# Performance work log

Hardware: AMD Instinct MI355X
Metric: run time of the kernel (lower is better)

The kernel has to match this reference:

```python
import jax, jax.numpy as jnp
import numpy as np
import math

EPS = 1e-6
ROPE_BASE = 10000.0

def _rmsnorm(x, w):
    # normalize over last dim (head_dim)
    rms = jax.lax.rsqrt(jnp.mean(x * x, axis=-1, keepdims=True) + EPS)
    return x * rms * w

def _rope_cos_sin(seq_len, head_dim, dtype):
    inv_freq = 1.0 / (ROPE_BASE ** (jnp.arange(0, head_dim, 2, dtype=jnp.float32) / head_dim))
    t = jnp.arange(seq_len, dtype=jnp.float32)
    freqs = jnp.outer(t, inv_freq)            # [S, Dh/2]
    emb = jnp.concatenate([freqs, freqs], -1)  # [S, Dh]
    return jnp.cos(emb).astype(dtype), jnp.sin(emb).astype(dtype)

def _rotate_half(x):
    half = x.shape[-1] // 2
    return jnp.concatenate([-x[..., half:], x[..., :half]], axis=-1)

def setup_inputs() -> dict:
    key = jax.random.key(0)
    ks = jax.random.split(key, 6)
    B, S, E = 1, 2048, 2048
    H, KVH, Dh = 16, 4, 128
    x = jax.random.normal(ks[0], (B, S, E), dtype=jnp.float32)
    mask = jnp.triu(jnp.ones((S, S), dtype=bool), k=1)  # True = masked (causal)
    scale = 0.02
    Wq = jax.random.normal(ks[1], (E, E), dtype=jnp.float32) * scale
    Wk = jax.random.normal(ks[2], (KVH * Dh, E), dtype=jnp.float32) * scale
    Wv = jax.random.normal(ks[3], (KVH * Dh, E), dtype=jnp.float32) * scale
    Wo = jax.random.normal(ks[4], (E, E), dtype=jnp.float32) * scale
    q_norm_w = jnp.ones((Dh,), dtype=jnp.float32)
    k_norm_w = jnp.ones((Dh,), dtype=jnp.float32)
    return {"x": x, "mask": mask, "Wq": Wq, "Wk": Wk, "Wv": Wv, "Wo": Wo,
            "q_norm_w": q_norm_w, "k_norm_w": k_norm_w}

def reference(x, mask, Wq, Wk, Wv, Wo, q_norm_w, k_norm_w):
    B, S, E = x.shape
    H, Dh = 16, E // 16
    KVH = Wk.shape[0] // Dh
    rep = H // KVH
    # QKV projections (torch Linear: x @ W.T)
    q = (x @ Wq.T).reshape(B, S, H, Dh).transpose(0, 2, 1, 3)    # [B,H,S,Dh]
    k = (x @ Wk.T).reshape(B, S, KVH, Dh).transpose(0, 2, 1, 3)  # [B,KVH,S,Dh]
    v = (x @ Wv.T).reshape(B, S, KVH, Dh).transpose(0, 2, 1, 3)
    # QK-RMSNorm
    q = _rmsnorm(q, q_norm_w)
    k = _rmsnorm(k, k_norm_w)
    # RoPE
    cos, sin = _rope_cos_sin(S, Dh, q.dtype)  # [S,Dh]
    q = q * cos + _rotate_half(q) * sin
    k = k * cos + _rotate_half(k) * sin
    # GQA expand kv heads (repeat_interleave on head dim)
    k = jnp.repeat(k, rep, axis=1)  # [B,H,S,Dh]
    v = jnp.repeat(v, rep, axis=1)
    # SDPA (no yarn => scale = 1/sqrt(head_dim))
    scale = 1.0 / math.sqrt(Dh)
    scores = jnp.einsum('bhqd,bhkd->bhqk', q, k) * scale
    scores = jnp.where(mask[None, None, :, :], -jnp.inf, scores)
    attn = jax.nn.softmax(scores, axis=-1)
    attn = jnp.nan_to_num(attn, nan=0.0)
    out = jnp.einsum('bhqk,bhkd->bhqd', attn, v)
    out = out.transpose(0, 2, 1, 3).reshape(B, S, E)
    return out @ Wo.T
```

## Files before the change

kernel.cpp:

```cpp
#include <hip/hip_runtime.h>
#include <hip/hip_bf16.h>
#include <cstdint>
#include <cstddef>

using bf16 = __hip_bfloat16;
typedef __attribute__((ext_vector_type(8))) short short8;
typedef __attribute__((ext_vector_type(4))) float f32x4;

#define MFMA16(a, b, c) __builtin_amdgcn_mfma_f32_16x16x32_bf16((a), (b), (c), 0, 0, 0)

static constexpr int S = 2048;
static constexpr int E = 2048;
static constexpr int H = 16;
static constexpr int KVH = 4;
static constexpr int Dh = 128;
static constexpr int NQKV = 3072;
static constexpr float ATTN_SCALE = 0.08838834764831845f;
static constexpr float NEG_BIG = -1e30f;

__device__ __forceinline__ short f2bs(float f) {
  __hip_bfloat16 h = __float2bfloat16(f);
  return *reinterpret_cast<short*>(&h);
}

__device__ __forceinline__ unsigned int pack_bf16(float lo, float hi) {
  return ((unsigned int)(unsigned short)f2bs(hi) << 16) |
         (unsigned int)(unsigned short)f2bs(lo);
}

__device__ __forceinline__ void gload_lds16(const void* g, void* l) {
  __builtin_amdgcn_global_load_lds(
      (const __attribute__((address_space(1))) unsigned int*)g,
      (__attribute__((address_space(3))) unsigned int*)l,
      16, 0, 0);
}

__global__ void cvt_all(const float* __restrict__ x,  const float* __restrict__ wq,
                        const float* __restrict__ wk, const float* __restrict__ wv,
                        const float* __restrict__ wo,
                        bf16* __restrict__ xb, bf16* __restrict__ wcat,
                        bf16* __restrict__ wob) {
  const long M1 = 4l << 20, M2 = 8l << 20, M3 = 9l << 20, M4 = 10l << 20, M5 = 14l << 20;
  long i = ((long)blockIdx.x * 256 + threadIdx.x) * 8;
  if (i >= M5) return;
  const float* src;
  bf16* dst;
  if (i < M1)      { src = x  + i;        dst = xb + i; }
  else if (i < M2) { src = wq + (i - M1); dst = wcat + (i - M1); }
  else if (i < M3) { src = wk + (i - M2); dst = wcat + 2048l * 2048 + (i - M2); }
  else if (i < M4) { src = wv + (i - M3); dst = wcat + 2560l * 2048 + (i - M3); }
  else             { src = wo + (i - M4); dst = wob + (i - M4); }
  const float4* s4 = reinterpret_cast<const float4*>(src);
  float4 a = s4[0];
  float4 b = s4[1];
  short8 o;
  o[0] = f2bs(a.x); o[1] = f2bs(a.y); o[2] = f2bs(a.z); o[3] = f2bs(a.w);
  o[4] = f2bs(b.x); o[5] = f2bs(b.y); o[6] = f2bs(b.z); o[7] = f2bs(b.w);
  *reinterpret_cast<short8*>(dst) = o;
}

template <bool OUT_F32>
__global__ __launch_bounds__(256, 2) void gemm_nt(const bf16* __restrict__ A,
                                                  const bf16* __restrict__ B,
                                                  void* __restrict__ Cout,
                                                  int M, int N, int K) {
  __shared__ bf16 As[128 * 32];
  __shared__ bf16 Bs[128 * 32];
  const int tid = threadIdx.x;
  const int lane = tid & 63;
  const int wv = tid >> 6;
  const int lr = lane & 15, lq = lane >> 4;
  const int wm = (wv >> 1) * 64, wn = (wv & 1) * 64;

  const int nwgx = M >> 7;
  const int nwg = (M >> 7) * (N >> 7);
  const int id = blockIdx.x + gridDim.x * blockIdx.y;
  const int sid = (id & 7) * (nwg >> 3) + (id >> 3);
  const int bm = (sid % nwgx) * 128, bn = (sid / nwgx) * 128;

  f32x4 acc[4][4] = {};

  for (int k0 = 0; k0 < K; k0 += 32) {
    __syncthreads();
    for (int it = 0; it < 2; ++it) {
      int ci = it * 256 + tid;
      int row = ci >> 2, co = (ci & 3) * 8;
      gload_lds16(A + (size_t)(bm + row) * K + k0 + co, As + (it * 256 + wv * 64) * 8);
      gload_lds16(B + (size_t)(bn + row) * K + k0 + co, Bs + (it * 256 + wv * 64) * 8);
    }
    __syncthreads();

    short8 af[4], bfr[4];
#pragma unroll
    for (int im = 0; im < 4; ++im)
      af[im] = *reinterpret_cast<const short8*>(As + (wm + im * 16 + lr) * 32 + lq * 8);
#pragma unroll
    for (int jn = 0; jn < 4; ++jn)
      bfr[jn] = *reinterpret_cast<const short8*>(Bs + (wn + jn * 16 + lr) * 32 + lq * 8);
#pragma unroll
    for (int im = 0; im < 4; ++im)
#pragma unroll
      for (int jn = 0; jn < 4; ++jn)
        acc[im][jn] = MFMA16(af[im], bfr[jn], acc[im][jn]);
  }

#pragma unroll
  for (int im = 0; im < 4; ++im)
#pragma unroll
    for (int jn = 0; jn < 4; ++jn)
#pragma unroll
      for (int i = 0; i < 4; ++i) {
        int r = bm + wm + im * 16 + lq * 4 + i;
        int c = bn + wn + jn * 16 + lr;
        if (OUT_F32)
          reinterpret_cast<float*>(Cout)[(size_t)r * N + c] = acc[im][jn][i];
        else
          reinterpret_cast<bf16*>(Cout)[(size_t)r * N + c] = __float2bfloat16(acc[im][jn][i]);
      }
}

__global__ __launch_bounds__(256, 2) void gemm_nt64(const bf16* __restrict__ A,
                                                    const bf16* __restrict__ B,
                                                    float* __restrict__ Cout,
                                                    int M, int N, int K) {
  __shared__ bf16 As[128 * 32];
  __shared__ bf16 Bs[64 * 32];
  const int tid = threadIdx.x;
  const int lane = tid & 63;
  const int wv = tid >> 6;
  const int lr = lane & 15, lq = lane >> 4;
  const int wm = (wv >> 1) * 64, wn = (wv & 1) * 32;

  const int nwgx = M >> 7;
  const int nwg = (M >> 7) * (N >> 6);
  const int id = blockIdx.x + gridDim.x * blockIdx.y;
  const int sid = (id & 7) * (nwg >> 3) + (id >> 3);
  const int bm = (sid % nwgx) * 128, bn = (sid / nwgx) * 64;

  f32x4 acc[4][2] = {};

  for (int k0 = 0; k0 < K; k0 += 32) {
    __syncthreads();
#pragma unroll
    for (int it = 0; it < 2; ++it) {
      int ci = it * 256 + tid;
      int row = ci >> 2, co = (ci & 3) * 8;
      gload_lds16(A + (size_t)(bm + row) * K + k0 + co, As + (it * 256 + wv * 64) * 8);
    }
    {
      int ci = tid;
      int row = ci >> 2, co = (ci & 3) * 8;
      gload_lds16(B + (size_t)(bn + row) * K + k0 + co, Bs + (wv * 64) * 8);
    }
    __syncthreads();

    short8 af[4], bfr[2];
#pragma unroll
    for (int im = 0; im < 4; ++im)
      af[im] = *reinterpret_cast<const short8*>(As + (wm + im * 16 + lr) * 32 + lq * 8);
#pragma unroll
    for (int jn = 0; jn < 2; ++jn)
      bfr[jn] = *reinterpret_cast<const short8*>(Bs + (wn + jn * 16 + lr) * 32 + lq * 8);
#pragma unroll
    for (int im = 0; im < 4; ++im)
#pragma unroll
      for (int jn = 0; jn < 2; ++jn)
        acc[im][jn] = MFMA16(af[im], bfr[jn], acc[im][jn]);
  }

#pragma unroll
  for (int im = 0; im < 4; ++im)
#pragma unroll
    for (int jn = 0; jn < 2; ++jn)
#pragma unroll
      for (int i = 0; i < 4; ++i) {
        int r = bm + wm + im * 16 + lq * 4 + i;
        int c = bn + wn + jn * 16 + lr;
        Cout[(size_t)r * N + c] = acc[im][jn][i];
      }
}

__global__ void qk_norm_rope_vt(const bf16* __restrict__ QKV,
                                const float* __restrict__ qw, const float* __restrict__ kw,
                                bf16* __restrict__ Qn, bf16* __restrict__ Kn,
                                bf16* __restrict__ Vt) {
  __shared__ bf16 t[64][65];
  if (blockIdx.x >= 10240) {
    const int vb = blockIdx.x - 10240;
    const int s0 = (vb & 31) * 64;
    const int c0 = (vb >> 5) * 64;
    const int kvh = c0 >> 7, d0 = c0 & 127;
#pragma unroll 4
    for (int i = 0; i < 16; ++i) {
      int lin = i * 256 + threadIdx.x;
      int r = lin >> 6, c = lin & 63;
      t[r][c] = QKV[(size_t)(s0 + r) * NQKV + 2560 + c0 + c];
    }
    __syncthreads();
#pragma unroll 4
    for (int i = 0; i < 16; ++i) {
      int lin = i * 256 + threadIdx.x;
      int d = lin >> 6, s = lin & 63;
      Vt[((size_t)kvh * 128 + d0 + d) * S + s0 + s] = t[s][d];
    }
    return;
  }

  const int lane = threadIdx.x & 63;
  const int w = threadIdx.x >> 6;
  const int row = blockIdx.x * 4 + w;
  const int s = row / 20;
  const int hh = row % 20;

  const bf16* src;
  bf16* dst;
  const float* wt;
  float outscale;
  if (hh < 16) {
    src = QKV + (size_t)s * NQKV + hh * Dh;
    dst = Qn + ((size_t)hh * S + s) * Dh;
    wt = qw;
    outscale = ATTN_SCALE;
  } else {
    int kvh = hh - 16;
    src = QKV + (size_t)s * NQKV + 2048 + kvh * Dh;
    dst = Kn + ((size_t)kvh * S + s) * Dh;
    wt = kw;
    outscale = 1.0f;
  }

  float x0 = __bfloat162float(src[lane]);
  float x1 = __bfloat162float(src[lane + 64]);
  float ss = x0 * x0 + x1 * x1;
#pragma unroll
  for (int off = 1; off < 64; off <<= 1) ss += __shfl_xor(ss, off);
  float rms = rsqrtf(ss * (1.0f / 128.0f) + 1e-6f);
  float n0 = x0 * rms * wt[lane];
  float n1 = x1 * rms * wt[lane + 64];

  float inv_freq = exp2f((float)lane * -0.2076205059304601f);
  float ang = (float)s * inv_freq;
  float sn, cs;
  sincosf(ang, &sn, &cs);
  float o0 = (n0 * cs - n1 * sn) * outscale;
  float o1 = (n1 * cs + n0 * sn) * outscale;
  dst[lane] = __float2bfloat16(o0);
  dst[lane + 64] = __float2bfloat16(o1);
}

__device__ __forceinline__ void chunk_decode(int u, int& qi, int& c, int& nc) {
  if (u < 8)       { qi = u;               c = 0;      nc = 1; }
  else if (u < 24) { int v = u - 8;  qi = 8  + (v >> 1); c = v & 1;  nc = 2; }
  else if (u < 48) { int v = u - 24; qi = 16 + v / 3;    c = v % 3;  nc = 3; }
  else             { int v = u - 48; qi = 24 + (v >> 2); c = v & 3;  nc = 4; }
}

__global__ __launch_bounds__(256, 2) void attn_fwd(const bf16* __restrict__ Qn,
                                                   const bf16* __restrict__ Kn,
                                                   const bf16* __restrict__ Vt,
                                                   bf16* __restrict__ AO,
                                                   bf16* __restrict__ Opart,
                                                   float* __restrict__ ml) {
  __shared__ bf16 Ks[2][64 * 128];
  __shared__ bf16 Vs[2][128 * 64];
  __shared__ bf16 Ps[4][16 * 64];

  const int tid = threadIdx.x;
  const int lane = tid & 63;
  const int w = tid >> 6;
  const int lr = lane & 15, lq = lane >> 4;

  const int bx = blockIdx.x;
  const int h = bx / 80, u = bx % 80;
  int qi, cch, nc;
  chunk_decode(u, qi, cch, nc);
  const int kvh = h >> 2;
  const int q0 = qi * 64;
  const int t0 = cch * 8;
  const int t1 = min(t0 + 8, qi + 1);

  const bf16* Qbase = Qn + ((size_t)h * S + q0 + w * 16) * Dh;
  const bf16* Kbase = Kn + (size_t)kvh * S * Dh;
  const bf16* Vbase = Vt + (size_t)kvh * Dh * S;
  char* Pw = (char*)&Ps[w][0];

  short8 qf[4];
#pragma unroll
  for (int dd = 0; dd < 4; ++dd)
    qf[dd] = *reinterpret_cast<const short8*>(Qbase + (size_t)lr * Dh + dd * 32 + lq * 8);

  short8 ones;
#pragma unroll
  for (int e = 0; e < 8; ++e) ones[e] = (short)0x3F80;

  float m = NEG_BIG;
  f32x4 lacc = {};
  f32x4 oacc[8] = {};

  auto stageK = [&](int tile, int b) {
    const int kb = tile * 64;
#pragma unroll
    for (int i = 0; i < 4; ++i) {
      int chunk = i * 256 + tid;
      int r = chunk >> 4, c = chunk & 15;
      int cs = c ^ (r & 7);
      gload_lds16(Kbase + (size_t)(kb + r) * Dh + cs * 8,
                  (bf16*)Ks + b * 8192 + (i * 256 + w * 64) * 8);
    }
  };
  auto stageV = [&](int tile, int b) {
    const int kb = tile * 64;
#pragma unroll
    for (int i = 0; i < 4; ++i) {
      int chunk = i * 256 + tid;
      int r = chunk >> 3, c = chunk & 7;
      int cs = c ^ (r & 7);
      gload_lds16(Vbase + (size_t)r * S + kb + cs * 8,
                  (bf16*)Vs + b * 8192 + (i * 256 + w * 64) * 8);
    }
  };

  stageK(t0, 0);
  stageV(t0, 0);
  __syncthreads();
  int buf = 0;

  for (int t = t0; t < t1; ++t) {
    if (t + 1 < t1) { stageK(t + 1, buf ^ 1); stageV(t + 1, buf ^ 1); }

    f32x4 sacc[4] = {};
    __builtin_amdgcn_s_setprio(1);
#pragma unroll
    for (int jn = 0; jn < 4; ++jn) {
      int r = jn * 16 + lr;
      const char* kroww = (const char*)Ks + buf * 16384 + r * 256;
      int rx = r & 7;
#pragma unroll
      for (int dd = 0; dd < 4; ++dd) {
        int cg = (dd * 4 + lq) ^ rx;
        short8 kf = *reinterpret_cast<const short8*>(kroww + cg * 16);
        sacc[jn] = MFMA16(kf, qf[dd], sacc[jn]);
      }
    }
    __builtin_amdgcn_s_setprio(0);

    const bool diag = (t == qi);
    float p[4][4];
    float pm = NEG_BIG;
#pragma unroll
    for (int jn = 0; jn < 4; ++jn)
#pragma unroll
      for (int i = 0; i < 4; ++i) {
        float v = sacc[jn][i];
        if (diag && (jn * 16 + lq * 4 + i > w * 16 + lr)) v = NEG_BIG;
        p[jn][i] = v;
        pm = fmaxf(pm, v);
      }
    pm = fmaxf(pm, __shfl_xor(pm, 16));
    pm = fmaxf(pm, __shfl_xor(pm, 32));

    if (!__all(pm - m <= 8.0f)) {
      float mnew = fmaxf(m, pm);
      float a = __expf(m - mnew);
      m = mnew;
      float aq[4];
#pragma unroll
      for (int i = 0; i < 4; ++i) aq[i] = __shfl(a, lq * 4 + i);
#pragma unroll
      for (int i = 0; i < 4; ++i) {
        lacc[i] *= aq[i];
#pragma unroll
        for (int jd = 0; jd < 8; ++jd) oacc[jd][i] *= aq[i];
      }
    }

    unsigned int wd[4][2];
#pragma unroll
    for (int jn = 0; jn < 4; ++jn)
#pragma unroll
      for (int uu = 0; uu < 2; ++uu) {
        float plo = __expf(p[jn][2 * uu] - m);
        float phi = __expf(p[jn][2 * uu + 1] - m);
        wd[jn][uu] = pack_bf16(plo, phi);
      }

#pragma unroll
    for (int jn = 0; jn < 4; ++jn) {
      int slot = jn * 2 + (lq >> 1);
      *reinterpret_cast<uint2*>(Pw + lr * 128 + ((slot ^ (lr & 7)) * 16 + (lq & 1) * 8)) =
          make_uint2(wd[jn][0], wd[jn][1]);
    }
    __builtin_amdgcn_wave_barrier();
    short8 pa[2];
#pragma unroll
    for (int kk = 0; kk < 2; ++kk) {
      int slot = kk * 4 + lq;
      pa[kk] = *reinterpret_cast<const short8*>(Pw + lr * 128 + ((slot ^ (lr & 7)) * 16));
    }

    __builtin_amdgcn_s_setprio(1);
#pragma unroll
    for (int kk = 0; kk < 2; ++kk) {
      lacc = MFMA16(pa[kk], ones, lacc);
#pragma unroll
      for (int jd = 0; jd < 8; ++jd) {
        int r = jd * 16 + lr;
        int cg = (kk * 4 + lq) ^ (r & 7);
        short8 vf = *reinterpret_cast<const short8*>((const char*)Vs + buf * 16384 + r * 128 + cg * 16);
        oacc[jd] = MFMA16(pa[kk], vf, oacc[jd]);
      }
    }
    __builtin_amdgcn_s_setprio(0);

    __syncthreads();
    buf ^= 1;
  }

  if (nc == 1) {
#pragma unroll
    for (int jd = 0; jd < 8; ++jd)
#pragma unroll
      for (int i = 0; i < 4; ++i) {
        float o = oacc[jd][i] / lacc[i];
        AO[(size_t)(q0 + w * 16 + lq * 4 + i) * E + h * Dh + jd * 16 + lr] = __float2bfloat16(o);
      }
  } else {
    const int pidx = h * 80 + u;
    bf16* Op = Opart + (size_t)pidx * 64 * 128;
#pragma unroll
    for (int jd = 0; jd < 8; ++jd)
#pragma unroll
      for (int i = 0; i < 4; ++i)
        Op[(w * 16 + lq * 4 + i) * 128 + jd * 16 + lr] = __float2bfloat16(oacc[jd][i]);
    if (lq == 0)
      ml[(size_t)pidx * 128 + (w * 16 + lr) * 2] = m;
    if (lr == 0) {
#pragma unroll
      for (int i = 0; i < 4; ++i)
        ml[(size_t)pidx * 128 + (w * 16 + lq * 4 + i) * 2 + 1] = lacc[i];
    }
  }
}

__global__ __launch_bounds__(256) void attn_combine(const bf16* __restrict__ Opart,
                                                    const float* __restrict__ ml,
                                                    bf16* __restrict__ AO) {
  const int qi = 8 + blockIdx.x;
  const int h = blockIdx.y;
  const int nc = qi / 8 + 1;
  const int off = (qi < 16) ? 8 + (qi - 8) * 2
                : (qi < 24) ? 24 + (qi - 16) * 3
                            : 48 + (qi - 24) * 4;
  const int base = h * 80 + off;
  const int row = threadIdx.x >> 2;
  const int d0 = (threadIdx.x & 3) * 32;

  float mc[4], lc[4];
  float M = -INFINITY;
  for (int c = 0; c < nc; ++c) {
    mc[c] = ml[(size_t)(base + c) * 128 + row * 2];
    lc[c] = ml[(size_t)(base + c) * 128 + row * 2 + 1];
    M = fmaxf(M, mc[c]);
  }
  float L = 0.0f;
  float acc[32];
#pragma unroll
  for (int j = 0; j < 32; ++j) acc[j] = 0.0f;
  for (int c = 0; c < nc; ++c) {
    float wgt = __expf(mc[c] - M);
    L += wgt * lc[c];
    const short8* op = reinterpret_cast<const short8*>(
        Opart + (size_t)(base + c) * 8192 + row * 128 + d0);
#pragma unroll
    for (int j4 = 0; j4 < 4; ++j4) {
      short8 vv = op[j4];
#pragma unroll
      for (int e = 0; e < 8; ++e) {
        short sv = vv[e];
        acc[j4 * 8 + e] += wgt * __bfloat162float(*reinterpret_cast<bf16*>(&sv));
      }
    }
  }
  float inv = 1.0f / L;
  bf16* ao = AO + (size_t)(qi * 64 + row) * E + h * Dh + d0;
  short8 outv[4];
#pragma unroll
  for (int j4 = 0; j4 < 4; ++j4) {
#pragma unroll
    for (int e = 0; e < 8; ++e) outv[j4][e] = f2bs(acc[j4 * 8 + e] * inv);
    reinterpret_cast<short8*>(ao)[j4] = outv[j4];
  }
}

extern "C" void kernel_launch(void* const* d_in, const int* in_sizes, int n_in,
                              void* d_out, int out_size, void* d_ws, size_t ws_size,
                              hipStream_t stream) {
  const float* x  = (const float*)d_in[0];
  const float* Wq = (const float*)d_in[2];
  const float* Wk = (const float*)d_in[3];
  const float* Wv = (const float*)d_in[4];
  const float* Wo = (const float*)d_in[5];
  const float* qw = (const float*)d_in[6];
  const float* kw = (const float*)d_in[7];

  char* ws = (char*)d_ws;
  bf16* xb   = (bf16*)(ws + (0ull << 20));
  bf16* Wcat = (bf16*)(ws + (8ull << 20));
  bf16* Wob  = (bf16*)(ws + (20ull << 20));
  bf16* QKV  = (bf16*)(ws + (28ull << 20));
  bf16* Qn   = (bf16*)(ws + (40ull << 20));
  bf16* Kn   = (bf16*)(ws + (48ull << 20));
  bf16* Vt   = (bf16*)(ws + (50ull << 20));
  bf16* AO   = (bf16*)(ws + (52ull << 20));
  bf16* Opart = (bf16*)(ws + (0ull << 20));
  float* ml   = (float*)(ws + (28ull << 20));

  cvt_all<<<7168, 256, 0, stream>>>(x, Wq, Wk, Wv, Wo, xb, Wcat, Wob);

  gemm_nt<false><<<dim3(S / 128, NQKV / 128), 256, 0, stream>>>(xb, Wcat, QKV, S, NQKV, E);

  qk_norm_rope_vt<<<10240 + 256, 256, 0, stream>>>(QKV, qw, kw, Qn, Kn, Vt);

  attn_fwd<<<16 * 80, 256, 0, stream>>>(Qn, Kn, Vt, AO, Opart, ml);
  attn_combine<<<dim3(24, 16), 256, 0, stream>>>(Opart, ml, AO);

  gemm_nt64<<<dim3(S / 128, E / 64), 256, 0, stream>>>(AO, Wob, (float*)d_out, S, E, E);
}
```

Before: 161.4 us.

## Double attention query tile to 128 rows per block and reorder blocks heavy-first

Each wave now handles 32 query rows (two 16-row halves) so every K/V tile staged in LDS is reused across twice as many queries, halving K/V global and LDS traffic per query. The split-KV chunking, partial-output layout and combine kernel are rescaled for 128-row query tiles. The block index is remapped so the heaviest (longest causal) chunks launch first and heads are interleaved. In exchange, register pressure roughly doubles (two sets of accumulators), and the block count halves, which may reduce occupancy and parallelism.

```diff
diff --git a/kernel.cpp b/kernel.cpp
--- a/kernel.cpp
+++ b/kernel.cpp
@@ -248,11 +248,11 @@
   dst[lane + 64] = __float2bfloat16(o1);
 }
 
-__device__ __forceinline__ void chunk_decode(int u, int& qi, int& c, int& nc) {
-  if (u < 8)       { qi = u;               c = 0;      nc = 1; }
-  else if (u < 24) { int v = u - 8;  qi = 8  + (v >> 1); c = v & 1;  nc = 2; }
-  else if (u < 48) { int v = u - 24; qi = 16 + v / 3;    c = v % 3;  nc = 3; }
-  else             { int v = u - 48; qi = 24 + (v >> 2); c = v & 3;  nc = 4; }
+__device__ __forceinline__ void chunk_decode128(int u, int& qt, int& c, int& nc) {
+  if (u < 4)       { qt = u;                c = 0;      nc = 1; }
+  else if (u < 12) { int v = u - 4;  qt = 4  + (v >> 1); c = v & 1;  nc = 2; }
+  else if (u < 24) { int v = u - 12; qt = 8  + v / 3;    c = v % 3;  nc = 3; }
+  else             { int v = u - 24; qt = 12 + (v >> 2); c = v & 3;  nc = 4; }
 }
 
 __global__ __launch_bounds__(256, 2) void attn_fwd(const bf16* __restrict__ Qn,
@@ -263,7 +263,7 @@
                                                    float* __restrict__ ml) {
   __shared__ bf16 Ks[2][64 * 128];
   __shared__ bf16 Vs[2][128 * 64];
-  __shared__ bf16 Ps[4][16 * 64];
+  __shared__ bf16 Ps[4][2][16 * 64];
 
   const int tid = threadIdx.x;
   const int lane = tid & 63;
@@ -271,31 +271,35 @@
   const int lr = lane & 15, lq = lane >> 4;
 
   const int bx = blockIdx.x;
-  const int h = bx / 80, u = bx % 80;
-  int qi, cch, nc;
-  chunk_decode(u, qi, cch, nc);
+  const int h = bx & 15;
+  const int u = 39 - (bx >> 4);
+  int qt, cch, nc;
+  chunk_decode128(u, qt, cch, nc);
   const int kvh = h >> 2;
-  const int q0 = qi * 64;
+  const int q0 = qt * 128;
   const int t0 = cch * 8;
-  const int t1 = min(t0 + 8, qi + 1);
-
-  const bf16* Qbase = Qn + ((size_t)h * S + q0 + w * 16) * Dh;
+  const int t1 = min(t0 + 8, 2 * qt + 2);
+
+  const bf16* Qbase = Qn + ((size_t)h * S + q0 + w * 32) * Dh;
   const bf16* Kbase = Kn + (size_t)kvh * S * Dh;
   const bf16* Vbase = Vt + (size_t)kvh * Dh * S;
-  char* Pw = (char*)&Ps[w][0];
-
-  short8 qf[4];
-#pragma unroll
-  for (int dd = 0; dd < 4; ++dd)
-    qf[dd] = *reinterpret_cast<const short8*>(Qbase + (size_t)lr * Dh + dd * 32 + lq * 8);
+  char* PwA = (char*)&Ps[w][0][0];
+  char* PwB = (char*)&Ps[w][1][0];
+
+  short8 qfA[4], qfB[4];
+#pragma unroll
+  for (int dd = 0; dd < 4; ++dd) {
+    qfA[dd] = *reinterpret_cast<const short8*>(Qbase + (size_t)lr * Dh + dd * 32 + lq * 8);
+    qfB[dd] = *reinterpret_cast<const short8*>(Qbase + (size_t)(16 + lr) * Dh + dd * 32 + lq * 8);
+  }
 
   short8 ones;
 #pragma unroll
   for (int e = 0; e < 8; ++e) ones[e] = (short)0x3F80;
 
-  float m = NEG_BIG;
-  f32x4 lacc = {};
-  f32x4 oacc[8] = {};
+  float mA = NEG_BIG, mB = NEG_BIG;
+  f32x4 laccA = {}, laccB = {};
+  f32x4 oaccA[8] = {}, oaccB[8] = {};
 
   auto stageK = [&](int tile, int b) {
     const int kb = tile * 64;
@@ -320,31 +324,9 @@
     }
   };
 
-  stageK(t0, 0);
-  stageV(t0, 0);
-  __syncthreads();
-  int buf = 0;
-
-  for (int t = t0; t < t1; ++t) {
-    if (t + 1 < t1) { stageK(t + 1, buf ^ 1); stageV(t + 1, buf ^ 1); }
-
-    f32x4 sacc[4] = {};
-    __builtin_amdgcn_s_setprio(1);
-#pragma unroll
-    for (int jn = 0; jn < 4; ++jn) {
-      int r = jn * 16 + lr;
-      const char* kroww = (const char*)Ks + buf * 16384 + r * 256;
-      int rx = r & 7;
-#pragma unroll
-      for (int dd = 0; dd < 4; ++dd) {
-        int cg = (dd * 4 + lq) ^ rx;
-        short8 kf = *reinterpret_cast<const short8*>(kroww + cg * 16);
-        sacc[jn] = MFMA16(kf, qf[dd], sacc[jn]);
-      }
-    }
-    __builtin_amdgcn_s_setprio(0);
-
-    const bool diag = (t == qi);
+  auto sm_half = [&](f32x4* sacc, float& m, f32x4& lacc, f32x4* oacc,
+                     int rowlo, char* Pwh, int kb) {
+    const bool needmask = (kb + 63 > rowlo);
     float p[4][4];
     float pm = NEG_BIG;
 #pragma unroll
@@ -352,13 +334,12 @@
 #pragma unroll
       for (int i = 0; i < 4; ++i) {
         float v = sacc[jn][i];
-        if (diag && (jn * 16 + lq * 4 + i > w * 16 + lr)) v = NEG_BIG;
+        if (needmask && (kb + jn * 16 + lq * 4 + i > rowlo + lr)) v = NEG_BIG;
         p[jn][i] = v;
         pm = fmaxf(pm, v);
       }
     pm = fmaxf(pm, __shfl_xor(pm, 16));
     pm = fmaxf(pm, __shfl_xor(pm, 32));
-
     if (!__all(pm - m <= 8.0f)) {
       float mnew = fmaxf(m, pm);
       float a = __expf(m - mnew);
@@ -373,41 +354,74 @@
         for (int jd = 0; jd < 8; ++jd) oacc[jd][i] *= aq[i];
       }
     }
-
-    unsigned int wd[4][2];
+    unsigned int wdv[4][2];
 #pragma unroll
     for (int jn = 0; jn < 4; ++jn)
 #pragma unroll
       for (int uu = 0; uu < 2; ++uu) {
         float plo = __expf(p[jn][2 * uu] - m);
         float phi = __expf(p[jn][2 * uu + 1] - m);
-        wd[jn][uu] = pack_bf16(plo, phi);
-      }
-
+        wdv[jn][uu] = pack_bf16(plo, phi);
+      }
 #pragma unroll
     for (int jn = 0; jn < 4; ++jn) {
       int slot = jn * 2 + (lq >> 1);
-      *reinterpret_cast<uint2*>(Pw + lr * 128 + ((slot ^ (lr & 7)) * 16 + (lq & 1) * 8)) =
-          make_uint2(wd[jn][0], wd[jn][1]);
-    }
+      *reinterpret_cast<uint2*>(Pwh + lr * 128 + ((slot ^ (lr & 7)) * 16 + (lq & 1) * 8)) =
+          make_uint2(wdv[jn][0], wdv[jn][1]);
+    }
+  };
+
+  stageK(t0, 0);
+  stageV(t0, 0);
+  __syncthreads();
+  int buf = 0;
+
+  for (int t = t0; t < t1; ++t) {
+    const int kb = t * 64;
+    if (t + 1 < t1) { stageK(t + 1, buf ^ 1); stageV(t + 1, buf ^ 1); }
+
+    f32x4 sA[4] = {}, sB[4] = {};
+    __builtin_amdgcn_s_setprio(1);
+#pragma unroll
+    for (int jn = 0; jn < 4; ++jn) {
+      int r = jn * 16 + lr;
+      const char* kroww = (const char*)Ks + buf * 16384 + r * 256;
+      int rx = r & 7;
+#pragma unroll
+      for (int dd = 0; dd < 4; ++dd) {
+        int cg = (dd * 4 + lq) ^ rx;
+        short8 kf = *reinterpret_cast<const short8*>(kroww + cg * 16);
+        sA[jn] = MFMA16(kf, qfA[dd], sA[jn]);
+        sB[jn] = MFMA16(kf, qfB[dd], sB[jn]);
+      }
+    }
+    __builtin_amdgcn_s_setprio(0);
+
+    sm_half(sA, mA, laccA, oaccA, q0 + w * 32,      PwA, kb);
+    sm_half(sB, mB, laccB, oaccB, q0 + w * 32 + 16, PwB, kb);
+
     __builtin_amdgcn_wave_barrier();
-    short8 pa[2];
+
+    short8 paA[2], paB[2];
 #pragma unroll
     for (int kk = 0; kk < 2; ++kk) {
-      int slot = kk * 4 + lq;
-      pa[kk] = *reinterpret_cast<const short8*>(Pw + lr * 128 + ((slot ^ (lr & 7)) * 16));
+      int so = ((kk * 4 + lq) ^ (lr & 7)) * 16;
+      paA[kk] = *reinterpret_cast<const short8*>(PwA + lr * 128 + so);
+      paB[kk] = *reinterpret_cast<const short8*>(PwB + lr * 128 + so);
     }
 
     __builtin_amdgcn_s_setprio(1);
 #pragma unroll
     for (int kk = 0; kk < 2; ++kk) {
-      lacc = MFMA16(pa[kk], ones, lacc);
+      laccA = MFMA16(paA[kk], ones, laccA);
+      laccB = MFMA16(paB[kk], ones, laccB);
 #pragma unroll
       for (int jd = 0; jd < 8; ++jd) {
         int r = jd * 16 + lr;
         int cg = (kk * 4 + lq) ^ (r & 7);
         short8 vf = *reinterpret_cast<const short8*>((const char*)Vs + buf * 16384 + r * 128 + cg * 16);
-        oacc[jd] = MFMA16(pa[kk], vf, oacc[jd]);
+        oaccA[jd] = MFMA16(paA[kk], vf, oaccA[jd]);
+        oaccB[jd] = MFMA16(paB[kk], vf, oaccB[jd]);
       }
     }
     __builtin_amdgcn_s_setprio(0);
@@ -421,23 +435,31 @@
     for (int jd = 0; jd < 8; ++jd)
 #pragma unroll
       for (int i = 0; i < 4; ++i) {
-        float o = oacc[jd][i] / lacc[i];
-        AO[(size_t)(q0 + w * 16 + lq * 4 + i) * E + h * Dh + jd * 16 + lr] = __float2bfloat16(o);
+        float oA = oaccA[jd][i] / laccA[i];
+        float oB = oaccB[jd][i] / laccB[i];
+        AO[(size_t)(q0 + w * 32 + lq * 4 + i) * E + h * Dh + jd * 16 + lr] = __float2bfloat16(oA);
+        AO[(size_t)(q0 + w * 32 + 16 + lq * 4 + i) * E + h * Dh + jd * 16 + lr] = __float2bfloat16(oB);
       }
   } else {
-    const int pidx = h * 80 + u;
-    bf16* Op = Opart + (size_t)pidx * 64 * 128;
+    const int pidx = h * 36 + (u - 4);
+    bf16* Op = Opart + (size_t)pidx * 128 * 128;
 #pragma unroll
     for (int jd = 0; jd < 8; ++jd)
 #pragma unroll
-      for (int i = 0; i < 4; ++i)
-        Op[(w * 16 + lq * 4 + i) * 128 + jd * 16 + lr] = __float2bfloat16(oacc[jd][i]);
-    if (lq == 0)
-      ml[(size_t)pidx * 128 + (w * 16 + lr) * 2] = m;
+      for (int i = 0; i < 4; ++i) {
+        Op[(w * 32 + lq * 4 + i) * 128 + jd * 16 + lr] = __float2bfloat16(oaccA[jd][i]);
+        Op[(w * 32 + 16 + lq * 4 + i) * 128 + jd * 16 + lr] = __float2bfloat16(oaccB[jd][i]);
+      }
+    if (lq == 0) {
+      ml[(size_t)pidx * 256 + (w * 32 + lr) * 2] = mA;
+      ml[(size_t)pidx * 256 + (w * 32 + 16 + lr) * 2] = mB;
+    }
     if (lr == 0) {
 #pragma unroll
-      for (int i = 0; i < 4; ++i)
-        ml[(size_t)pidx * 128 + (w * 16 + lq * 4 + i) * 2 + 1] = lacc[i];
+      for (int i = 0; i < 4; ++i) {
+        ml[(size_t)pidx * 256 + (w * 32 + lq * 4 + i) * 2 + 1] = laccA[i];
+        ml[(size_t)pidx * 256 + (w * 32 + 16 + lq * 4 + i) * 2 + 1] = laccB[i];
+      }
     }
   }
 }
@@ -445,21 +467,21 @@
 __global__ __launch_bounds__(256) void attn_combine(const bf16* __restrict__ Opart,
                                                     const float* __restrict__ ml,
                                                     bf16* __restrict__ AO) {
-  const int qi = 8 + blockIdx.x;
+  const int qt = 4 + blockIdx.x;
   const int h = blockIdx.y;
-  const int nc = qi / 8 + 1;
-  const int off = (qi < 16) ? 8 + (qi - 8) * 2
-                : (qi < 24) ? 24 + (qi - 16) * 3
-                            : 48 + (qi - 24) * 4;
-  const int base = h * 80 + off;
-  const int row = threadIdx.x >> 2;
+  const int nc = (qt < 8) ? 2 : (qt < 12) ? 3 : 4;
+  const int off4 = (qt < 8) ? (qt - 4) * 2
+                 : (qt < 12) ? 8 + (qt - 8) * 3
+                             : 20 + (qt - 12) * 4;
+  const int base = h * 36 + off4;
+  const int row = blockIdx.z * 64 + (threadIdx.x >> 2);
   const int d0 = (threadIdx.x & 3) * 32;
 
   float mc[4], lc[4];
   float M = -INFINITY;
   for (int c = 0; c < nc; ++c) {
-    mc[c] = ml[(size_t)(base + c) * 128 + row * 2];
-    lc[c] = ml[(size_t)(base + c) * 128 + row * 2 + 1];
+    mc[c] = ml[(size_t)(base + c) * 256 + row * 2];
+    lc[c] = ml[(size_t)(base + c) * 256 + row * 2 + 1];
     M = fmaxf(M, mc[c]);
   }
   float L = 0.0f;
@@ -470,7 +492,7 @@
     float wgt = __expf(mc[c] - M);
     L += wgt * lc[c];
     const short8* op = reinterpret_cast<const short8*>(
-        Opart + (size_t)(base + c) * 8192 + row * 128 + d0);
+        Opart + (size_t)(base + c) * 16384 + row * 128 + d0);
 #pragma unroll
     for (int j4 = 0; j4 < 4; ++j4) {
       short8 vv = op[j4];
@@ -482,7 +504,7 @@
     }
   }
   float inv = 1.0f / L;
-  bf16* ao = AO + (size_t)(qi * 64 + row) * E + h * Dh + d0;
+  bf16* ao = AO + (size_t)(qt * 128 + row) * E + h * Dh + d0;
   short8 outv[4];
 #pragma unroll
   for (int j4 = 0; j4 < 4; ++j4) {
@@ -521,8 +543,8 @@
 
   qk_norm_rope_vt<<<10240 + 256, 256, 0, stream>>>(QKV, qw, kw, Qn, Kn, Vt);
 
-  attn_fwd<<<16 * 80, 256, 0, stream>>>(Qn, Kn, Vt, AO, Opart, ml);
-  attn_combine<<<dim3(24, 16), 256, 0, stream>>>(Opart, ml, AO);
+  attn_fwd<<<640, 256, 0, stream>>>(Qn, Kn, Vt, AO, Opart, ml);
+  attn_combine<<<dim3(12, 16, 2), 256, 0, stream>>>(Opart, ml, AO);
 
   gemm_nt64<<<dim3(S / 128, E / 64), 256, 0, stream>>>(AO, Wob, (float*)d_out, S, E, E);
 }
```

Measured after the change: 162.3 us. No clear change (+0.6%).
